# Kernel tuning notes

Hardware: AMD Instinct MI355X
Metric: run time of the kernel (lower is better)

## Reference

```python
import jax, jax.numpy as jnp
import numpy as np

ALPHA = 0.2  # LeakyReLU negative slope

def setup_inputs() -> dict:
    key = jax.random.key(0)
    k1, k2, k3 = jax.random.split(key, 3)
    B, N, F, H = 2, 4096, 512, 8
    d = F // H  # per-head in/out dim = 64
    h = jax.random.normal(k1, (B, N, F), dtype=jnp.float32)
    # xavier-uniform-like scale (gain 1.414, fan 64+64)
    W = jax.random.normal(k2, (H, d, d), dtype=jnp.float32) * 0.15
    a = jax.random.normal(k3, (H, 2 * d), dtype=jnp.float32) * 0.15
    return {"h": h, "W": W, "a": a}

def reference(h, W, a):
    B, N, F = h.shape
    H, _, o = W.shape
    d = F // H
    # split features per head: [B, H, N, d]
    hh = h.reshape(B, N, H, d).transpose(0, 2, 1, 3)
    Wh = jnp.einsum('bhnd,hdo->bhno', hh, W)          # [B,H,N,o]
    a1, a2 = a[:, :o], a[:, o:]
    Wh1 = jnp.einsum('bhno,ho->bhn', Wh, a1)          # [B,H,N]
    Wh2 = jnp.einsum('bhno,ho->bhn', Wh, a2)          # [B,H,N]
    e = jax.nn.leaky_relu(Wh1[..., :, None] + Wh2[..., None, :], ALPHA)  # [B,H,N,N]
    att = jax.nn.softmax(e, axis=-1)
    h_prime = jnp.einsum('bhnm,bhmo->bhno', att, Wh)  # [B,H,N,o]
    out = jax.nn.elu(h_prime)                         # concat=True -> ELU
    # concat heads along feature dim: [B, N, H*o]
    return out.transpose(0, 2, 1, 3).reshape(B, N, H * o)
```

## Files before the change

### kernel.cpp

```cpp
#include <hip/hip_runtime.h>
#include <hip/hip_fp16.h>


#define NB   2
#define NN   4096
#define NH   8
#define ALPHA 0.2f
#define LOG2E 1.4426950408889634f

typedef _Float16 f16x8 __attribute__((ext_vector_type(8)));
typedef _Float16 f16x2 __attribute__((ext_vector_type(2)));
typedef float    f32x4 __attribute__((ext_vector_type(4)));

__device__ __forceinline__ float dot2acc(f16x2 a, f16x2 b, float c) {
#if __has_builtin(__builtin_amdgcn_fdot2)
    return __builtin_amdgcn_fdot2(a, b, c, false);
#else
    return c + (float)a[0] * (float)b[0] + (float)a[1] * (float)b[1];
#endif
}

__global__ __launch_bounds__(256) void k_wh(
    const float* __restrict__ hsrc, const float* __restrict__ W,
    const float* __restrict__ a,
    _Float16* __restrict__ Wh_p, float* __restrict__ fb, float* __restrict__ gb)
{
    const int bid  = blockIdx.x;
    const int tile = bid & 63;
    const int bh   = bid >> 6;
    const int hh   = bh & 7;
    const int b    = bh >> 3;
    const int n0   = tile * 64;
    const int t    = threadIdx.x;

    __shared__ float Wl[64 * 68];
    __shared__ float ht[64 * 68];
    __shared__ float red[2 * 64 * 16];

    {
        const float* Wg = W + hh * 4096;
        #pragma unroll
        for (int p = 0; p < 4; p++) {
            int idx = (t + p * 256) * 4;
            float4 v = *(const float4*)(Wg + idx);
            int k = idx >> 6, c = idx & 63;
            *(float4*)(&Wl[k * 68 + c]) = v;
        }
    }
    {
        #pragma unroll
        for (int p = 0; p < 4; p++) {
            int idx = t + p * 256;
            int r = idx >> 4, kq = (idx & 15) * 4;
            float4 v = *(const float4*)(hsrc + ((size_t)(b * NN + n0 + r)) * 512 + hh * 64 + kq);
            *(float4*)(&ht[r * 68 + kq]) = v;
        }
    }
    __syncthreads();

    const int rq = t >> 4, cq = t & 15;
    float acc[4][4] = {};
    for (int k4 = 0; k4 < 64; k4 += 4) {
        float4 hv[4], wv[4];
        #pragma unroll
        for (int i = 0; i < 4; i++) hv[i] = *(const float4*)(&ht[(rq * 4 + i) * 68 + k4]);
        #pragma unroll
        for (int kk = 0; kk < 4; kk++) wv[kk] = *(const float4*)(&Wl[(k4 + kk) * 68 + cq * 4]);
        #pragma unroll
        for (int i = 0; i < 4; i++) {
            const float* hp = (const float*)&hv[i];
            #pragma unroll
            for (int kk = 0; kk < 4; kk++) {
                const float* wp = (const float*)&wv[kk];
                #pragma unroll
                for (int j = 0; j < 4; j++)
                    acc[i][j] = fmaf(hp[kk], wp[j], acc[i][j]);
            }
        }
    }

    float a1v[4], a2v[4];
    {
        const float* ag = a + hh * 128;
        #pragma unroll
        for (int j = 0; j < 4; j++) { a1v[j] = ag[cq * 4 + j]; a2v[j] = ag[64 + cq * 4 + j]; }
    }
    __syncthreads();

    _Float16* wt = (_Float16*)ht;
    #pragma unroll
    for (int i = 0; i < 4; i++) {
        float fp = 0.f, gp = 0.f;
        #pragma unroll
        for (int j = 0; j < 4; j++) {
            fp = fmaf(acc[i][j], a1v[j], fp);
            gp = fmaf(acc[i][j], a2v[j], gp);
        }
        red[0 * 1024 + (rq * 4 + i) * 16 + cq] = fp;
        red[1 * 1024 + (rq * 4 + i) * 16 + cq] = gp;
        #pragma unroll
        for (int j = 0; j < 4; j++)
            wt[(cq * 4 + j) * 72 + rq * 4 + i] = (_Float16)acc[i][j];
    }
    __syncthreads();

    if (t < 128) {
        int which = t >> 6, row = t & 63;
        const float* rr = &red[which * 1024 + row * 16];
        float s = 0.f;
        #pragma unroll
        for (int j = 0; j < 16; j++) s += rr[j];
        s *= LOG2E;
        float* dst = which ? gb : fb;
        dst[(size_t)bh * NN + n0 + row] = s;
    }

    #pragma unroll
    for (int p = 0; p < 2; p++) {
        int idx = t + p * 256;
        int ms  = idx >> 8;
        int ct  = (idx >> 6) & 3;
        int l   = idx & 63;
        f16x8 v = *(const f16x8*)(&wt[(ct * 16 + (l & 15)) * 72 + ms * 32 + (l >> 4) * 8]);
        *(f16x8*)(Wh_p + (size_t)bh * 64 * NN
                       + (((size_t)(tile * 2 + ms) * 4 + ct) * 64 + l) * 8) = v;
    }
}

__global__ __launch_bounds__(256) void k_prep(const float* __restrict__ gball,
                                              float* __restrict__ G,
                                              char* __restrict__ egfg_base)
{
    int bh = blockIdx.x, t = threadIdx.x;
    const float* g = gball + (size_t)bh * NN;
    float vals[16];
    float m = -1e30f;
    #pragma unroll
    for (int j = 0; j < 16; j++) { vals[j] = g[t + j * 256]; m = fmaxf(m, vals[j]); }
    #pragma unroll
    for (int s = 1; s < 64; s <<= 1) m = fmaxf(m, __shfl_xor(m, s, 64));
    __shared__ float wm[4];
    if ((t & 63) == 0) wm[t >> 6] = m;
    __syncthreads();
    float Gv = fmaxf(fmaxf(wm[0], wm[1]), fmaxf(wm[2], wm[3]));
    if (t == 0) G[bh] = Gv;
    _Float16* Eg = (_Float16*)(egfg_base + (size_t)bh * 16384);
    _Float16* Fg = Eg + NN;
    #pragma unroll
    for (int j = 0; j < 16; j++) {
        int i = t + j * 256;
        float d = vals[j] - Gv;
        Eg[i] = (_Float16)exp2f(d);
        Fg[i] = (_Float16)exp2f(ALPHA * d);
    }
}

__global__ __launch_bounds__(256, 3) void k_attn(
    const _Float16* __restrict__ Wh_p, const float* __restrict__ fb,
    const float* __restrict__ G, const char* __restrict__ egfg_base,
    float* __restrict__ out)
{
    const int orig  = blockIdx.x;
    const int bid   = (orig & 7) * 64 + (orig >> 3);
    const int ntile = bid & 31;
    const int bh    = bid >> 5;
    const int hh    = bh & 7;
    const int b     = bh >> 3;
    const int n0    = ntile * 128;
    const int t     = threadIdx.x;
    const int w     = t >> 6;
    const int l     = t & 63;
    const int kg    = w >> 1;
    const int wr    = w & 1;
    const int lr    = l & 15;
    const int lg    = l >> 4;

    const _Float16* Pp  = Wh_p + (size_t)bh * 64 * NN;
    const _Float16* Egp = (const _Float16*)(egfg_base + (size_t)bh * 16384);
    const float     Gv  = G[bh];

    f16x2 ef2[4], ff2[4];
    #pragma unroll
    for (int rg = 0; rg < 4; rg++) {
        int rn = n0 + wr * 64 + rg * 16 + lr;
        float s  = fb[(size_t)bh * NN + rn] + Gv;
        float t1 = (1.f - ALPHA) * s;
        _Float16 e = (_Float16)exp2f(fminf(t1, 0.f));
        _Float16 f = (_Float16)exp2f(fminf(-t1, 0.f));
        ef2[rg] = (f16x2){e, e};
        ff2[rg] = (f16x2){f, f};
    }
    const f16x2 one2 = (f16x2){(_Float16)1.0f, (_Float16)1.0f};

    f32x4 acc[4][4];
    #pragma unroll
    for (int rg = 0; rg < 4; rg++)
        #pragma unroll
        for (int ct = 0; ct < 4; ct++) acc[rg][ct] = (f32x4){0.f, 0.f, 0.f, 0.f};
    float dsum[4] = {0.f, 0.f, 0.f, 0.f};

    const _Float16* bp  = Pp + (size_t)kg * 64 * 2048 + (size_t)l * 8;
    const _Float16* ep  = Egp + kg * 2048 + lg * 8;
    const _Float16* epf = ep + NN;

    #define LOADSET(B0,B1,B2,B3,EG,FG)                                          \
        {                                                                        \
            B0 = *(const f16x8*)(bp);         B1 = *(const f16x8*)(bp + 512);    \
            B2 = *(const f16x8*)(bp + 1024);  B3 = *(const f16x8*)(bp + 1536);   \
            EG = *(const f16x8*)ep;           FG = *(const f16x8*)epf;           \
            bp += 2048; ep += 32; epf += 32;                                     \
        }

    #define COMPUTE(B0,B1,B2,B3,EG,FG)                                          \
        {                                                                        \
            _Pragma("unroll")                                                    \
            for (int rg = 0; rg < 4; rg++) {                                     \
                f16x8 af; float ds = dsum[rg];                                   \
                _Pragma("unroll")                                                \
                for (int d = 0; d < 4; d++) {                                    \
                    f16x2 e2 = ((const f16x2*)&(EG))[d];                         \
                    f16x2 f2 = ((const f16x2*)&(FG))[d];                         \
                    f16x2 p2 = __builtin_elementwise_max(e2 * ef2[rg],           \
                                                         f2 * ff2[rg]);          \
                    ((f16x2*)&af)[d] = p2;                                       \
                    ds = dot2acc(p2, one2, ds);                                  \
                }                                                                \
                dsum[rg] = ds;                                                   \
                acc[rg][0] = __builtin_amdgcn_mfma_f32_16x16x32_f16(             \
                    af, B0, acc[rg][0], 0, 0, 0);                                \
                acc[rg][1] = __builtin_amdgcn_mfma_f32_16x16x32_f16(             \
                    af, B1, acc[rg][1], 0, 0, 0);                                \
                acc[rg][2] = __builtin_amdgcn_mfma_f32_16x16x32_f16(             \
                    af, B2, acc[rg][2], 0, 0, 0);                                \
                acc[rg][3] = __builtin_amdgcn_mfma_f32_16x16x32_f16(             \
                    af, B3, acc[rg][3], 0, 0, 0);                                \
            }                                                                    \
        }

    f16x8 a0, a1, a2, a3, ae, az;
    f16x8 c0, c1, c2, c3, ce, cz;
    LOADSET(a0, a1, a2, a3, ae, az);

    #pragma clang loop unroll(disable)
    for (int hs = 0; hs < 64; hs += 2) {
        LOADSET(c0, c1, c2, c3, ce, cz);
        COMPUTE(a0, a1, a2, a3, ae, az);
        if (hs + 2 < 64) LOADSET(a0, a1, a2, a3, ae, az);
        COMPUTE(c0, c1, c2, c3, ce, cz);
    }
    #undef LOADSET
    #undef COMPUTE

    __shared__ f32x4 __attribute__((aligned(16))) Rw[2][16 * 64];
    __shared__ float dnP[256];
    __shared__ float dnS[128];

    #pragma unroll
    for (int rg = 0; rg < 4; rg++) {
        float d = dsum[rg];
        d += __shfl_xor(d, 16, 64);
        d += __shfl_xor(d, 32, 64);
        if (lg == 0) dnP[kg * 128 + wr * 64 + rg * 16 + lr] = d;
    }

    if (kg == 1) {
        #pragma unroll
        for (int rg = 0; rg < 4; rg++)
            #pragma unroll
            for (int ct = 0; ct < 4; ct++)
                Rw[wr][(rg * 4 + ct) * 64 + l] = acc[rg][ct];
    }
    __syncthreads();

    if (kg == 0) {
        dnS[wr * 64 + l] = dnP[wr * 64 + l] + dnP[128 + wr * 64 + l];
        float* outp = out + ((size_t)(b * NN + n0)) * 512 + hh * 64;
        #pragma unroll
        for (int rg = 0; rg < 4; rg++)
            #pragma unroll
            for (int reg = 0; reg < 4; reg++) {
                int row = wr * 64 + rg * 16 + lg * 4 + reg;
                float rinv = 1.0f / dnS[row];
                #pragma unroll
                for (int ct = 0; ct < 4; ct++) {
                    float v = (acc[rg][ct][reg] + Rw[wr][(rg * 4 + ct) * 64 + l][reg])
                              * rinv;
                    v = v > 0.f ? v : (exp2f(v * LOG2E) - 1.f);
                    outp[(size_t)row * 512 + ct * 16 + lr] = v;
                }
            }
    }
}

extern "C" void kernel_launch(void* const* d_in, const int* in_sizes, int n_in,
                              void* d_out, int out_size, void* d_ws, size_t ws_size,
                              hipStream_t stream)
{
    const float* hsrc = (const float*)d_in[0];
    const float* W    = (const float*)d_in[1];
    const float* a    = (const float*)d_in[2];
    float* outp       = (float*)d_out;

    const size_t WHT_BYTES = (size_t)NB * NH * 64 * NN * sizeof(_Float16);
    const size_t FB_BYTES  = (size_t)NB * NH * NN * sizeof(float);
    const size_t GB_BYTES  = (size_t)NB * NH * NN * sizeof(float);
    const size_t NEED = WHT_BYTES + FB_BYTES + GB_BYTES + 64 * sizeof(float);
    if (ws_size < NEED) return;

    char* ws = (char*)d_ws;
    _Float16* Wh_p = (_Float16*)ws;
    float*    fbuf = (float*)(ws + WHT_BYTES);
    char*     gbase = ws + WHT_BYTES + FB_BYTES;
    float*    Gmax = (float*)(ws + WHT_BYTES + FB_BYTES + GB_BYTES);

    k_wh  <<<dim3(NB * NH * (NN / 64)),  dim3(256), 0, stream>>>(hsrc, W, a, Wh_p, fbuf, (float*)gbase);
    k_prep<<<dim3(NB * NH),              dim3(256), 0, stream>>>((const float*)gbase, Gmax, gbase);
    k_attn<<<dim3(NB * NH * (NN / 128)), dim3(256), 0, stream>>>(Wh_p, fbuf, Gmax, gbase, outp);
}
```

Baseline: 65.40 us.

## Split attention key range across four wave groups with 512-thread blocks

Doubles k_attn block size to 512 threads so four wave groups each process a quarter of the key dimension instead of two halves. This shortens each wave's serial MFMA loop and raises latency hiding per block. In exchange, the cross-group reduction of accumulators goes through shared memory serially, which adds several extra barriers, and the launch bound of 4 may force register pressure or spills for the 64-float accumulator.

```diff
diff --git a/kernel.cpp b/kernel.cpp
--- a/kernel.cpp
+++ b/kernel.cpp
@@ -155,7 +155,7 @@
     }
 }
 
-__global__ __launch_bounds__(256, 3) void k_attn(
+__global__ __launch_bounds__(512, 4) void k_attn(
     const _Float16* __restrict__ Wh_p, const float* __restrict__ fb,
     const float* __restrict__ G, const char* __restrict__ egfg_base,
     float* __restrict__ out)
@@ -199,8 +199,8 @@
         for (int ct = 0; ct < 4; ct++) acc[rg][ct] = (f32x4){0.f, 0.f, 0.f, 0.f};
     float dsum[4] = {0.f, 0.f, 0.f, 0.f};
 
-    const _Float16* bp  = Pp + (size_t)kg * 64 * 2048 + (size_t)l * 8;
-    const _Float16* ep  = Egp + kg * 2048 + lg * 8;
+    const _Float16* bp  = Pp + (size_t)kg * 32 * 2048 + (size_t)l * 8;
+    const _Float16* ep  = Egp + kg * 1024 + lg * 8;
     const _Float16* epf = ep + NN;
 
     #define LOADSET(B0,B1,B2,B3,EG,FG)                                          \
@@ -242,17 +242,17 @@
     LOADSET(a0, a1, a2, a3, ae, az);
 
     #pragma clang loop unroll(disable)
-    for (int hs = 0; hs < 64; hs += 2) {
+    for (int hs = 0; hs < 32; hs += 2) {
         LOADSET(c0, c1, c2, c3, ce, cz);
         COMPUTE(a0, a1, a2, a3, ae, az);
-        if (hs + 2 < 64) LOADSET(a0, a1, a2, a3, ae, az);
+        if (hs + 2 < 32) LOADSET(a0, a1, a2, a3, ae, az);
         COMPUTE(c0, c1, c2, c3, ce, cz);
     }
     #undef LOADSET
     #undef COMPUTE
 
     __shared__ f32x4 __attribute__((aligned(16))) Rw[2][16 * 64];
-    __shared__ float dnP[256];
+    __shared__ float dnP[512];
     __shared__ float dnS[128];
 
     #pragma unroll
@@ -263,17 +263,29 @@
         if (lg == 0) dnP[kg * 128 + wr * 64 + rg * 16 + lr] = d;
     }
 
-    if (kg == 1) {
-        #pragma unroll
-        for (int rg = 0; rg < 4; rg++)
-            #pragma unroll
-            for (int ct = 0; ct < 4; ct++)
-                Rw[wr][(rg * 4 + ct) * 64 + l] = acc[rg][ct];
-    }
+    #define WRITE_R()                                                            \
+        { _Pragma("unroll") for (int rg = 0; rg < 4; rg++)                       \
+          _Pragma("unroll") for (int ct = 0; ct < 4; ct++)                       \
+            Rw[wr][(rg * 4 + ct) * 64 + l] = acc[rg][ct]; }
+    #define ADD_R()                                                              \
+        { _Pragma("unroll") for (int rg = 0; rg < 4; rg++)                       \
+          _Pragma("unroll") for (int ct = 0; ct < 4; ct++)                       \
+            acc[rg][ct] += Rw[wr][(rg * 4 + ct) * 64 + l]; }
+
+    if (kg == 1) WRITE_R();
+    __syncthreads();
+    if (t < 128) dnS[t] = dnP[t] + dnP[128 + t] + dnP[256 + t] + dnP[384 + t];
+    if (kg == 0) ADD_R();
+    __syncthreads();
+    if (kg == 2) WRITE_R();
+    __syncthreads();
+    if (kg == 0) ADD_R();
+    __syncthreads();
+    if (kg == 3) WRITE_R();
     __syncthreads();
 
     if (kg == 0) {
-        dnS[wr * 64 + l] = dnP[wr * 64 + l] + dnP[128 + wr * 64 + l];
+        ADD_R();
         float* outp = out + ((size_t)(b * NN + n0)) * 512 + hh * 64;
         #pragma unroll
         for (int rg = 0; rg < 4; rg++)
@@ -283,13 +295,14 @@
                 float rinv = 1.0f / dnS[row];
                 #pragma unroll
                 for (int ct = 0; ct < 4; ct++) {
-                    float v = (acc[rg][ct][reg] + Rw[wr][(rg * 4 + ct) * 64 + l][reg])
-                              * rinv;
+                    float v = acc[rg][ct][reg] * rinv;
                     v = v > 0.f ? v : (exp2f(v * LOG2E) - 1.f);
                     outp[(size_t)row * 512 + ct * 16 + lr] = v;
                 }
             }
     }
+    #undef WRITE_R
+    #undef ADD_R
 }
 
 extern "C" void kernel_launch(void* const* d_in, const int* in_sizes, int n_in,
@@ -315,5 +328,5 @@
 
     k_wh  <<<dim3(NB * NH * (NN / 64)),  dim3(256), 0, stream>>>(hsrc, W, a, Wh_p, fbuf, (float*)gbase);
     k_prep<<<dim3(NB * NH),              dim3(256), 0, stream>>>((const float*)gbase, Gmax, gbase);
-    k_attn<<<dim3(NB * NH * (NN / 128)), dim3(256), 0, stream>>>(Wh_p, fbuf, Gmax, gbase, outp);
-}
+    k_attn<<<dim3(NB * NH * (NN / 128)), dim3(512), 0, stream>>>(Wh_p, fbuf, Gmax, gbase, outp);
+}
```

Measured after the change: 148.8 us. 2.28x slower.
